# Performance work log

Measured on AMD Instinct MI355X. Metric: run time of the kernel, lower is better.

## Reference

```python
import jax, jax.numpy as jnp
import numpy as np

B, S, D, E, H, TOPK = 4, 1024, 512, 8, 1536, 2
NORM_EPS = 1e-5

def _ln(x, w, b, eps=1e-5):
    m = jnp.mean(x, -1, keepdims=True)
    v = jnp.var(x, -1, keepdims=True)  # biased var, as torch LayerNorm
    return (x - m) * jax.lax.rsqrt(v + eps) * w + b

def _modulate(x, shift, scale):
    return x * (1 + scale[:, None, :]) + shift[:, None, :]

def setup_inputs() -> dict:
    key = jax.random.key(0)
    ks = jax.random.split(key, 14)
    s = 0.02
    return dict(
        x=jax.random.normal(ks[0], (B, S, D), jnp.float32),
        c=jax.random.normal(ks[1], (B, D), jnp.float32),
        W_ada=jax.random.normal(ks[2], (D, 6 * D), jnp.float32) * s,
        b_ada=jax.random.normal(ks[3], (6 * D,), jnp.float32) * 0.1,
        Wq=jax.random.normal(ks[4], (D, D), jnp.float32) * s,
        Wk=jax.random.normal(ks[5], (D, D), jnp.float32) * s,
        Wv=jax.random.normal(ks[6], (D, D), jnp.float32) * s,
        Wo=jax.random.normal(ks[7], (D, D), jnp.float32) * s,
        qn_w=jnp.ones((D,), jnp.float32), qn_b=jnp.zeros((D,), jnp.float32),
        kn_w=jnp.ones((D,), jnp.float32), kn_b=jnp.zeros((D,), jnp.float32),
        an_w=jnp.ones((D,), jnp.float32), an_b=jnp.zeros((D,), jnp.float32),
        fn_w=jnp.ones((D,), jnp.float32), fn_b=jnp.zeros((D,), jnp.float32),
        Wr=jax.random.normal(ks[8], (D, E), jnp.float32) * s,
        br=jnp.zeros((E,), jnp.float32),
        W1=jax.random.normal(ks[9], (E, D, H), jnp.float32) * s,
        W2=jax.random.normal(ks[10], (E, H, D), jnp.float32) * s,
        W3=jax.random.normal(ks[11], (E, D, H), jnp.float32) * s,
    )

def reference(x, c, W_ada, b_ada, Wq, Wk, Wv, Wo, qn_w, qn_b, kn_w, kn_b,
              an_w, an_b, fn_w, fn_b, Wr, br, W1, W2, W3):
    # adaLN conditioning: SiLU -> Linear -> 6 chunks
    mods = jax.nn.silu(c) @ W_ada + b_ada          # (B, 6D)
    sh_msa, sc_msa, g_msa, sh_mlp, sc_mlp, g_mlp = jnp.split(mods, 6, axis=1)

    # Attention (source attends over the FEATURE dim: scores are (B, D, D))
    h = _modulate(_ln(x, an_w, an_b, NORM_EPS), sh_msa, sc_msa)
    q = _ln(h @ Wq, qn_w, qn_b)
    k = _ln(h @ Wk, kn_w, kn_b)
    v = h @ Wv
    scores = jnp.einsum('bsd,bse->bde', q, k)      # (B, D, D), no 1/sqrt scale (as source)
    A = jax.nn.softmax(scores, axis=-1)
    attn = jnp.einsum('bde,bse->bsd', A, v) @ Wo   # (B, S, D)
    x = x + g_msa[:, None, :] * attn

    # MoE feed-forward (top-2 routing; output REPLACES x, no residual/gate per source)
    xm = _modulate(_ln(x, fn_w, fn_b, NORM_EPS), sh_mlp, sc_mlp)
    logits = xm @ Wr + br                          # (B, S, E)
    # F.normalize default dim=1 -> L2 normalize over the SEQUENCE axis (faithful)
    nrm = jnp.sqrt(jnp.sum(logits * logits, axis=1, keepdims=True))
    logits = logits / jnp.maximum(nrm, 1e-12)
    probs = jax.nn.softmax(logits, axis=-1)        # (B, S, E)
    vals, idx = jax.lax.top_k(probs, TOPK)

    T = B * S
    xf = xm.reshape(T, D)
    # dense combine weights: zero for unselected experts (same math as gather/scatter-add)
    wden = jnp.zeros((T, E), xf.dtype).at[jnp.arange(T)[:, None], idx.reshape(T, TOPK)].set(vals.reshape(T, TOPK))
    h1 = jnp.einsum('td,edh->teh', xf, W1)
    h3 = jnp.einsum('td,edh->teh', xf, W3)
    y = jnp.einsum('teh,ehd->ted', jnp.sin(h1) * h3, W2)  # sin-gated FFN per expert
    moe = jnp.einsum('ted,te->td', y, wden).reshape(B, S, D)

    avg = probs.mean(axis=0)                       # mean over batch dim only (faithful): (S, E)
    aux = jnp.sum((1.0 / E - avg) ** 2)
    return moe, aux
```

## Files before the change

### kernel.cpp

```cpp
#include <hip/hip_runtime.h>
#include <math.h>

#define NB 4
#define NS 1024
#define ND 512
#define NE 8
#define NH 1536
#define NT 4096
#define D6 3072

typedef _Float16 half_t;
typedef _Float16 f16x8 __attribute__((ext_vector_type(8)));
typedef _Float16 f16x4 __attribute__((ext_vector_type(4)));
typedef float    f32x4 __attribute__((ext_vector_type(4)));

#define LDC 136
#define TM_MAX 71

__device__ __forceinline__ void gld16(const void* g, void* l) {
  __builtin_amdgcn_global_load_lds((const __attribute__((address_space(1))) char*)g,
                                   (__attribute__((address_space(3))) char*)l, 16, 0, 0);
}

__device__ __forceinline__ int resolve_tile(const int* __restrict__ offs, int t,
                                            int& e_out, int& m0_out) {
  int acc = 0, found = 0, ee = 0, mm = 0;
  #pragma unroll
  for (int q = 0; q < NE; ++q) {
    int ne_q = offs[q + 1] - offs[q];
    int te = (ne_q + 127) >> 7;
    if (!found && t < acc + te) { ee = q; mm = (t - acc) << 7; found = 1; }
    acc += te;
  }
  e_out = ee; m0_out = mm;
  return found;
}

__global__ __launch_bounds__(256) void k_ada(const float* __restrict__ c,
    const float* __restrict__ Wada, const float* __restrict__ bada,
    float* __restrict__ mods)
{
  __shared__ float sc[ND];
  __shared__ float part[256];
  int tid = threadIdx.x;
  int blk = blockIdx.x;
  int o0 = blk * 64;
  int b = o0 / D6;
  int j0 = o0 - b * D6;
  for (int d = tid; d < ND; d += 256) {
    float v = c[b * ND + d];
    sc[d] = v / (1.f + expf(-v));
  }
  __syncthreads();
  int j = j0 + (tid & 63);
  int kc = tid >> 6;
  float acc = 0.f;
  #pragma unroll 8
  for (int d = kc * 128; d < kc * 128 + 128; ++d)
    acc += sc[d] * Wada[(size_t)d * D6 + j];
  part[tid] = acc;
  __syncthreads();
  if (tid < 64) {
    float r = part[tid] + part[tid + 64] + part[tid + 128] + part[tid + 192]
            + bada[j0 + tid];
    mods[b * D6 + j0 + tid] = r;
  }
}

__global__ __launch_bounds__(256) void k_lnmod(const float* X, int xstride,
    float* Yf, half_t* Yh, half_t* Yl, int ystride,
    const float* __restrict__ w, const float* __restrict__ b,
    const float* __restrict__ mods, int sh_off, int sc_off,
    const float* __restrict__ Wr, const float* __restrict__ br,
    float* __restrict__ logits)
{
  __shared__ float red[16];
  __shared__ float red2[32];
  int tid = threadIdx.x;
  int row = blockIdx.x;
  int batch = row >> 10;
  const float* xr = X + (size_t)row * xstride;
  float x0 = xr[tid], x1 = xr[tid + 256];
  float s = x0 + x1, q = x0 * x0 + x1 * x1;
  #pragma unroll
  for (int off = 32; off > 0; off >>= 1) { s += __shfl_down(s, off, 64); q += __shfl_down(q, off, 64); }
  if ((tid & 63) == 0) { red[tid >> 6] = s; red[8 + (tid >> 6)] = q; }
  __syncthreads();
  if (tid == 0) {
    float S = red[0] + red[1] + red[2] + red[3];
    float Q = red[8] + red[9] + red[10] + red[11];
    float mean = S * (1.f / (float)ND);
    float var = Q * (1.f / (float)ND) - mean * mean;
    red[0] = mean; red[1] = rsqrtf(var + 1e-5f);
  }
  __syncthreads();
  float mean = red[0], rstd = red[1];
  int d0 = tid, d1 = tid + 256;
  float y0 = (x0 - mean) * rstd * w[d0] + b[d0];
  float y1 = (x1 - mean) * rstd * w[d1] + b[d1];
  if (mods) {
    const float* mb = mods + batch * D6;
    y0 = y0 * (1.f + mb[sc_off + d0]) + mb[sh_off + d0];
    y1 = y1 * (1.f + mb[sc_off + d1]) + mb[sh_off + d1];
  }
  size_t o0 = (size_t)row * ystride + d0, o1 = (size_t)row * ystride + d1;
  if (Yf) { Yf[o0] = y0; Yf[o1] = y1; }
  if (Yh) {
    half_t h0 = (half_t)y0, h1 = (half_t)y1;
    Yh[o0] = h0; Yh[o1] = h1;
    if (Yl) { Yl[o0] = (half_t)(y0 - (float)h0); Yl[o1] = (half_t)(y1 - (float)h1); }
  }
  if (Wr) {
    float p[8];
    float4 wa = *(const float4*)(Wr + d0 * 8);
    float4 wb = *(const float4*)(Wr + d0 * 8 + 4);
    float4 wc = *(const float4*)(Wr + d1 * 8);
    float4 wd = *(const float4*)(Wr + d1 * 8 + 4);
    p[0] = y0 * wa.x + y1 * wc.x; p[1] = y0 * wa.y + y1 * wc.y;
    p[2] = y0 * wa.z + y1 * wc.z; p[3] = y0 * wa.w + y1 * wc.w;
    p[4] = y0 * wb.x + y1 * wd.x; p[5] = y0 * wb.y + y1 * wd.y;
    p[6] = y0 * wb.z + y1 * wd.z; p[7] = y0 * wb.w + y1 * wd.w;
    #pragma unroll
    for (int off = 32; off > 0; off >>= 1)
      #pragma unroll
      for (int e = 0; e < 8; ++e) p[e] += __shfl_down(p[e], off, 64);
    if ((tid & 63) == 0) {
      #pragma unroll
      for (int e = 0; e < 8; ++e) red2[(tid >> 6) * 8 + e] = p[e];
    }
    __syncthreads();
    if (tid < 8)
      logits[(size_t)row * 8 + tid] = red2[tid] + red2[8 + tid] + red2[16 + tid]
                                    + red2[24 + tid] + br[tid];
  }
}

__global__ __launch_bounds__(256) void k_lnqk(float* QKV,
    const float* __restrict__ qw, const float* __restrict__ qb,
    const float* __restrict__ kw, const float* __restrict__ kb)
{
  __shared__ float red[16];
  int tid = threadIdx.x;
  int row = blockIdx.x >> 1;
  int h = blockIdx.x & 1;
  const float* w = h ? kw : qw;
  const float* b = h ? kb : qb;
  float* xr = QKV + (size_t)row * 1536 + h * 512;
  float x0 = xr[tid], x1 = xr[tid + 256];
  float s = x0 + x1, q = x0 * x0 + x1 * x1;
  #pragma unroll
  for (int off = 32; off > 0; off >>= 1) { s += __shfl_down(s, off, 64); q += __shfl_down(q, off, 64); }
  if ((tid & 63) == 0) { red[tid >> 6] = s; red[8 + (tid >> 6)] = q; }
  __syncthreads();
  if (tid == 0) {
    float S = red[0] + red[1] + red[2] + red[3];
    float Q = red[8] + red[9] + red[10] + red[11];
    float mean = S * (1.f / (float)ND);
    float var = Q * (1.f / (float)ND) - mean * mean;
    red[0] = mean; red[1] = rsqrtf(var + 1e-5f);
  }
  __syncthreads();
  float mean = red[0], rstd = red[1];
  xr[tid]       = (x0 - mean) * rstd * w[tid] + b[tid];
  xr[tid + 256] = (x1 - mean) * rstd * w[tid + 256] + b[tid + 256];
}

__global__ __launch_bounds__(256) void k_tsplit2(const float* __restrict__ QKV,
    half_t* __restrict__ H0, half_t* __restrict__ L0)
{
  __shared__ float tile[32][33];
  int z = blockIdx.z;
  half_t* outH = H0 + (size_t)z * 4194304;
  half_t* outL = L0 + (size_t)z * 4194304;
  int col0 = z * 512;
  int s0 = blockIdx.x * 32, c0 = blockIdx.y * 32;
  int tid = threadIdx.x;
  int r = tid >> 5, c = tid & 31;
  #pragma unroll
  for (int p = 0; p < 4; ++p)
    tile[r + p * 8][c] = QKV[(size_t)(s0 + r + p * 8) * 1536 + col0 + c0 + c];
  __syncthreads();
  #pragma unroll
  for (int p = 0; p < 4; ++p) {
    float v = tile[c][r + p * 8];
    half_t h = (half_t)v;
    size_t o = (size_t)(c0 + r + p * 8) * NT + s0 + c;
    outH[o] = h; outL[o] = (half_t)(v - (float)h);
  }
}

__global__ __launch_bounds__(256) void k_wsplit4(const float* __restrict__ Wq,
    const float* __restrict__ Wk, const float* __restrict__ Wv,
    const float* __restrict__ Wo, half_t* __restrict__ outH, half_t* __restrict__ outL)
{
  __shared__ float tile[32][33];
  int z = blockIdx.z;
  const float* W = (z == 0) ? Wq : (z == 1) ? Wk : (z == 2) ? Wv : Wo;
  int rowoff = z * 512;
  int k0 = blockIdx.x * 32, n0 = blockIdx.y * 32;
  int tid = threadIdx.x;
  int r = tid >> 5, c = tid & 31;
  #pragma unroll
  for (int p = 0; p < 4; ++p)
    tile[r + p * 8][c] = W[(size_t)(k0 + r + p * 8) * ND + n0 + c];
  __syncthreads();
  #pragma unroll
  for (int p = 0; p < 4; ++p) {
    float v = tile[c][r + p * 8];
    half_t h = (half_t)v;
    size_t o = (size_t)(rowoff + n0 + r + p * 8) * ND + k0 + c;
    outH[o] = h; outL[o] = (half_t)(v - (float)h);
  }
}

__global__ __launch_bounds__(256) void k_vsplit(const float* __restrict__ QKV,
    half_t* __restrict__ Vh, half_t* __restrict__ Vl)
{
  int i = blockIdx.x * 256 + threadIdx.x;
  int s = i >> 7, c = (i & 127) * 4;
  float4 v = *(const float4*)(QKV + (size_t)s * 1536 + 1024 + c);
  f16x4 h, l;
  h[0] = (half_t)v.x; l[0] = (half_t)(v.x - (float)h[0]);
  h[1] = (half_t)v.y; l[1] = (half_t)(v.y - (float)h[1]);
  h[2] = (half_t)v.z; l[2] = (half_t)(v.z - (float)h[2]);
  h[3] = (half_t)v.w; l[3] = (half_t)(v.w - (float)h[3]);
  *(f16x4*)(Vh + (size_t)s * ND + c) = h;
  *(f16x4*)(Vl + (size_t)s * ND + c) = l;
}

template<int MODE>
__global__ __launch_bounds__(256, 2) void k_gemm_hl(
    const half_t* __restrict__ Ah, const half_t* __restrict__ Al, long long sAz,
    const half_t* __restrict__ Bh, const half_t* __restrict__ Bl, long long sBz,
    int lda, int ldb, int K,
    float* __restrict__ Cf, half_t* __restrict__ Ch, half_t* __restrict__ Cl,
    long long sCz, int ldc,
    const float* __restrict__ xres, const float* __restrict__ mods)
{
  int z = blockIdx.z;
  int m0 = blockIdx.x * 128, n0 = blockIdx.y * 128;
  __shared__ __align__(16) char smem[65536];
  half_t* Sh = (half_t*)smem;
  int tid = threadIdx.x;
  int lane = tid & 63, w = tid >> 6;
  int wm = (w >> 1) * 64, wn = (w & 1) * 64;
  int qd = lane >> 4, md = lane & 15;
  int rA0 = tid >> 2;
  int sw = (((tid & 3) ^ ((tid >> 3) & 3)) << 3);

  const half_t* pAh0 = Ah + z * sAz + (size_t)(m0 + rA0) * lda + sw;
  const half_t* pAh1 = pAh0 + (size_t)64 * lda;
  const half_t* pAl0 = Al + z * sAz + (size_t)(m0 + rA0) * lda + sw;
  const half_t* pAl1 = pAl0 + (size_t)64 * lda;
  const half_t* pBh0 = Bh + z * sBz + (size_t)(n0 + rA0) * ldb + sw;
  const half_t* pBh1 = pBh0 + (size_t)64 * ldb;
  const half_t* pBl0 = Bl + z * sBz + (size_t)(n0 + rA0) * ldb + sw;
  const half_t* pBl1 = pBl0 + (size_t)64 * ldb;

  char* dAh = smem + w * 1024;
  char* dAl = smem + 16384 + w * 1024;
  char* dBh = smem + 32768 + w * 1024;
  char* dBl = smem + 49152 + w * 1024;

  f32x4 acc[4][4];
  #pragma unroll
  for (int i = 0; i < 4; ++i)
    #pragma unroll
    for (int j = 0; j < 4; ++j)
      #pragma unroll
      for (int p = 0; p < 4; ++p) acc[i][j][p] = 0.f;

  int swq  = ((qd ^ ((md >> 1) & 3)) << 3);
  int aoff = (wm + md) * 32 + swq;
  int boff = (wn + md) * 32 + swq;

#define GEMM_STAGE(p, kk) do { int kb_ = (kk); int pb_ = (p) * 8192;         \
    gld16(pAh0 + kb_, dAh + pb_); gld16(pAh1 + kb_, dAh + pb_ + 4096);       \
    gld16(pAl0 + kb_, dAl + pb_); gld16(pAl1 + kb_, dAl + pb_ + 4096);       \
    gld16(pBh0 + kb_, dBh + pb_); gld16(pBh1 + kb_, dBh + pb_ + 4096);       \
    gld16(pBl0 + kb_, dBl + pb_); gld16(pBl1 + kb_, dBl + pb_ + 4096); } while (0)

  int iters = K >> 5;
  GEMM_STAGE(0, 0);
  int cur = 0;
  #pragma unroll 1
  for (int it = 0; it < iters; ++it) {
    if (it + 1 < iters) {
      GEMM_STAGE(cur ^ 1, (it + 1) * 32);
      asm volatile("s_waitcnt vmcnt(8)\ns_barrier" ::: "memory");
    } else {
      asm volatile("s_waitcnt vmcnt(0)\ns_barrier" ::: "memory");
    }
    const half_t* Ash = Sh + cur * 4096;
    const half_t* Asl = Sh + 8192  + cur * 4096;
    const half_t* Bsh = Sh + 16384 + cur * 4096;
    const half_t* Bsl = Sh + 24576 + cur * 4096;
    f16x8 ah[4], al[4], bh[4], bl[4];
    #pragma unroll
    for (int i = 0; i < 4; ++i) {
      ah[i] = *(const f16x8*)(Ash + aoff + i * 512);
      al[i] = *(const f16x8*)(Asl + aoff + i * 512);
    }
    #pragma unroll
    for (int j = 0; j < 4; ++j) {
      bh[j] = *(const f16x8*)(Bsh + boff + j * 512);
      bl[j] = *(const f16x8*)(Bsl + boff + j * 512);
    }
    __builtin_amdgcn_s_setprio(1);
    #pragma unroll
    for (int i = 0; i < 4; ++i)
      #pragma unroll
      for (int j = 0; j < 4; ++j) {
        acc[i][j] = __builtin_amdgcn_mfma_f32_16x16x32_f16(ah[i], bh[j], acc[i][j], 0, 0, 0);
        acc[i][j] = __builtin_amdgcn_mfma_f32_16x16x32_f16(ah[i], bl[j], acc[i][j], 0, 0, 0);
        acc[i][j] = __builtin_amdgcn_mfma_f32_16x16x32_f16(al[i], bh[j], acc[i][j], 0, 0, 0);
      }
    __builtin_amdgcn_s_setprio(0);
    asm volatile("s_barrier" ::: "memory");
    cur ^= 1;
  }
#undef GEMM_STAGE

  if (MODE == 1) {
    half_t* Cs = (half_t*)smem;
    __syncthreads();
    #pragma unroll
    for (int i = 0; i < 4; ++i)
      #pragma unroll
      for (int j = 0; j < 4; ++j)
        #pragma unroll
        for (int p = 0; p < 4; ++p)
          Cs[(wm + 16 * i + qd * 4 + p) * LDC + wn + 16 * j + md] = (half_t)acc[i][j][p];
    __syncthreads();
    #pragma unroll
    for (int it2 = 0; it2 < 8; ++it2) {
      int chunk = it2 * 256 + tid;
      int r = chunk >> 4, c8 = (chunk & 15) * 8;
      *(f16x8*)(Ch + z * sCz + (size_t)(m0 + r) * ldc + n0 + c8) = *(const f16x8*)(Cs + r * LDC + c8);
    }
    __syncthreads();
    #pragma unroll
    for (int i = 0; i < 4; ++i)
      #pragma unroll
      for (int j = 0; j < 4; ++j)
        #pragma unroll
        for (int p = 0; p < 4; ++p) {
          float v = acc[i][j][p];
          half_t h = (half_t)v;
          Cs[(wm + 16 * i + qd * 4 + p) * LDC + wn + 16 * j + md] = (half_t)(v - (float)h);
        }
    __syncthreads();
    #pragma unroll
    for (int it2 = 0; it2 < 8; ++it2) {
      int chunk = it2 * 256 + tid;
      int r = chunk >> 4, c8 = (chunk & 15) * 8;
      *(f16x8*)(Cl + z * sCz + (size_t)(m0 + r) * ldc + n0 + c8) = *(const f16x8*)(Cs + r * LDC + c8);
    }
  } else {
    #pragma unroll
    for (int i = 0; i < 4; ++i)
      #pragma unroll
      for (int p = 0; p < 4; ++p) {
        int r = m0 + wm + 16 * i + qd * 4 + p;
        float* cp = Cf + z * sCz + (size_t)r * ldc + n0 + wn + md;
        if (MODE == 2) {
          int batch = r >> 10;
          const float* mb = mods + batch * D6 + 2 * ND;
          const float* xp = xres + (size_t)r * ldc + n0 + wn + md;
          #pragma unroll
          for (int j = 0; j < 4; ++j) {
            int col = wn + md + 16 * j;
            cp[16 * j] = xp[16 * j] + mb[n0 + col] * acc[i][j][p];
          }
        } else {
          #pragma unroll
          for (int j = 0; j < 4; ++j) cp[16 * j] = acc[i][j][p];
        }
      }
  }
}

__global__ __launch_bounds__(256) void k_softmax512_sum4(const float* __restrict__ SC4,
    half_t* __restrict__ Ph, half_t* __restrict__ Pl)
{
  __shared__ float red[16];
  int tid = threadIdx.x;
  int row = blockIdx.x;
  int b = row >> 9, d = row & 511;
  const float* r0 = SC4 + ((size_t)(b * 4 + 0) << 18) + (size_t)d * ND;
  const float* r1 = SC4 + ((size_t)(b * 4 + 1) << 18) + (size_t)d * ND;
  const float* r2 = SC4 + ((size_t)(b * 4 + 2) << 18) + (size_t)d * ND;
  const float* r3 = SC4 + ((size_t)(b * 4 + 3) << 18) + (size_t)d * ND;
  float x0 = r0[tid] + r1[tid] + r2[tid] + r3[tid];
  float x1 = r0[tid + 256] + r1[tid + 256] + r2[tid + 256] + r3[tid + 256];
  float m = fmaxf(x0, x1);
  #pragma unroll
  for (int off = 32; off > 0; off >>= 1) m = fmaxf(m, __shfl_down(m, off, 64));
  if ((tid & 63) == 0) red[tid >> 6] = m;
  __syncthreads();
  if (tid == 0) red[0] = fmaxf(fmaxf(red[0], red[1]), fmaxf(red[2], red[3]));
  __syncthreads();
  m = red[0];
  float e0 = expf(x0 - m), e1 = expf(x1 - m);
  float s = e0 + e1;
  #pragma unroll
  for (int off = 32; off > 0; off >>= 1) s += __shfl_down(s, off, 64);
  if ((tid & 63) == 0) red[8 + (tid >> 6)] = s;
  __syncthreads();
  if (tid == 0) red[8] = red[8] + red[9] + red[10] + red[11];
  __syncthreads();
  float inv = 1.f / red[8];
  float p0 = e0 * inv, p1 = e1 * inv;
  size_t base = (size_t)row * ND;
  half_t h0 = (half_t)p0, h1 = (half_t)p1;
  Ph[base + tid] = h0;       Pl[base + tid] = (half_t)(p0 - (float)h0);
  Ph[base + tid + 256] = h1; Pl[base + tid + 256] = (half_t)(p1 - (float)h1);
}

__global__ __launch_bounds__(256) void k_colnorm(const float* __restrict__ logits,
    float* __restrict__ nrm, int* __restrict__ cnt)
{
  __shared__ float red[8];
  int tid = threadIdx.x;
  if (blockIdx.x == 0 && tid < 16) cnt[tid] = 0;
  int b = blockIdx.x >> 3, e = blockIdx.x & 7;
  float acc = 0.f;
  for (int s = tid; s < NS; s += 256) {
    float l = logits[((size_t)(b << 10) + s) * NE + e];
    acc += l * l;
  }
  #pragma unroll
  for (int off = 32; off > 0; off >>= 1) acc += __shfl_down(acc, off, 64);
  if ((tid & 63) == 0) red[tid >> 6] = acc;
  __syncthreads();
  if (tid == 0) nrm[b * NE + e] = sqrtf(red[0] + red[1] + red[2] + red[3]);
}

__global__ __launch_bounds__(256) void k_top2(const float* __restrict__ logits,
    const float* __restrict__ nrm, float* __restrict__ probs,
    float* __restrict__ wsel, int* __restrict__ isel, int* __restrict__ cnt)
{
  int t = blockIdx.x * 256 + threadIdx.x;
  int b = t >> 10;
  float p[NE];
  float mx = -1e30f;
  #pragma unroll
  for (int e = 0; e < NE; ++e) {
    float l = logits[t * NE + e] / fmaxf(nrm[b * NE + e], 1e-12f);
    p[e] = l;
    mx = fmaxf(mx, l);
  }
  float s = 0.f;
  #pragma unroll
  for (int e = 0; e < NE; ++e) { p[e] = expf(p[e] - mx); s += p[e]; }
  float inv = 1.f / s;
  #pragma unroll
  for (int e = 0; e < NE; ++e) { p[e] *= inv; probs[t * NE + e] = p[e]; }
  int i1 = 0;
  #pragma unroll
  for (int e = 1; e < NE; ++e) if (p[e] > p[i1]) i1 = e;
  int i2 = (i1 == 0) ? 1 : 0;
  #pragma unroll
  for (int e = 0; e < NE; ++e) if (e != i1 && p[e] > p[i2]) i2 = e;
  wsel[t * 2] = p[i1]; wsel[t * 2 + 1] = p[i2];
  isel[t * 2] = i1;    isel[t * 2 + 1] = i2;
  atomicAdd(&cnt[i1], 1); atomicAdd(&cnt[i2], 1);
}

__global__ void k_scan(const int* __restrict__ cnt, int* __restrict__ offs)
{
  if (threadIdx.x == 0) {
    int a = 0;
    for (int e = 0; e < NE; ++e) { offs[e] = a; a += cnt[e]; }
    offs[NE] = a;
  }
}

__global__ __launch_bounds__(256) void k_fill(const int* __restrict__ isel,
    const int* __restrict__ offs, int* __restrict__ cnt2,
    int* __restrict__ list, int* __restrict__ inv)
{
  int idx = blockIdx.x * 256 + threadIdx.x;
  int e = isel[idx];
  int pos = atomicAdd(&cnt2[e], 1);
  int slot = offs[e] + pos;
  list[slot] = idx >> 1;
  inv[idx] = slot;
}

__global__ __launch_bounds__(256) void k_aux(const float* __restrict__ probs,
    float* __restrict__ outAux)
{
  __shared__ float red[8];
  int tid = threadIdx.x;
  float acc = 0.f;
  for (int s = tid; s < NS; s += 256) {
    #pragma unroll
    for (int e = 0; e < NE; ++e) {
      float a = probs[(size_t)s * NE + e] + probs[(size_t)(NS + s) * NE + e]
              + probs[(size_t)(2 * NS + s) * NE + e] + probs[(size_t)(3 * NS + s) * NE + e];
      float d = 0.125f - a * 0.25f;
      acc += d * d;
    }
  }
  #pragma unroll
  for (int off = 32; off > 0; off >>= 1) acc += __shfl_down(acc, off, 64);
  if ((tid & 63) == 0) red[tid >> 6] = acc;
  __syncthreads();
  if (tid == 0) *outAux = red[0] + red[1] + red[2] + red[3];
}

__global__ __launch_bounds__(256) void k_tcast13(const float* __restrict__ W1,
    const float* __restrict__ W3, half_t* __restrict__ W1t, half_t* __restrict__ W3t)
{
  __shared__ float tile[32][33];
  int z = blockIdx.z;
  int sel = z >> 3, e = z & 7;
  const float* We = (sel ? W3 : W1) + (size_t)e * ND * NH;
  half_t* Wte = (sel ? W3t : W1t) + (size_t)e * ND * NH;
  int k0 = blockIdx.x * 32, n0 = blockIdx.y * 32;
  int tid = threadIdx.x;
  int r = tid >> 5, c = tid & 31;
  #pragma unroll
  for (int p = 0; p < 4; ++p)
    tile[r + p * 8][c] = We[(size_t)(k0 + r + p * 8) * NH + n0 + c];
  __syncthreads();
  #pragma unroll
  for (int p = 0; p < 4; ++p)
    Wte[(size_t)(n0 + r + p * 8) * ND + k0 + c] = (half_t)tile[c][r + p * 8];
}

__global__ __launch_bounds__(256) void k_tcastW2(const float* __restrict__ W,
    half_t* __restrict__ Wt)
{
  __shared__ float tile[32][33];
  const float* We = W + (size_t)blockIdx.z * NH * ND;
  half_t* Wte = Wt + (size_t)blockIdx.z * NH * ND;
  int k0 = blockIdx.x * 32, n0 = blockIdx.y * 32;
  int tid = threadIdx.x;
  int r = tid >> 5, c = tid & 31;
  #pragma unroll
  for (int p = 0; p < 4; ++p)
    tile[r + p * 8][c] = We[(size_t)(k0 + r + p * 8) * ND + n0 + c];
  __syncthreads();
  #pragma unroll
  for (int p = 0; p < 4; ++p)
    Wte[(size_t)(n0 + r + p * 8) * NH + k0 + c] = (half_t)tile[c][r + p * 8];
}

__global__ __launch_bounds__(256, 3) void k_ffn_fused(const half_t* __restrict__ xmh,
    const half_t* __restrict__ W1t, const half_t* __restrict__ W3t,
    const int* __restrict__ list, const int* __restrict__ offs,
    half_t* __restrict__ gate)
{
  int bx = blockIdx.x;
  int n0 = (bx % 12) * 128;
  int t  = bx / 12;
  int e, m0;
  if (!resolve_tile(offs, t, e, m0)) return;
  int base = offs[e], ne = offs[e + 1] - base;

  __shared__ __align__(16) char smem[49664];
  half_t* Sh = (half_t*)smem;
  int* rowt = (int*)(smem + 49152);
  int tid = threadIdx.x;
  if (tid < 128) {
    int rr = m0 + tid;
    rowt[tid] = (rr < ne) ? list[base + rr] : 0;
  }
  __syncthreads();

  int lane = tid & 63, w = tid >> 6;
  int wm = (w >> 1) * 64, wn = (w & 1) * 64;
  int qd = lane >> 4, md = lane & 15;
  int rA0 = tid >> 2;
  int sw = (((tid & 3) ^ ((tid >> 3) & 3)) << 3);
  int tok0 = rowt[rA0], tok1 = rowt[rA0 + 64];

  const half_t* gA0  = xmh + (size_t)tok0 * ND + sw;
  const half_t* gA1  = xmh + (size_t)tok1 * ND + sw;
  const half_t* gB10 = W1t + ((size_t)e * NH + n0 + rA0) * ND + sw;
  const half_t* gB11 = gB10 + (size_t)64 * ND;
  const half_t* gB30 = W3t + ((size_t)e * NH + n0 + rA0) * ND + sw;
  const half_t* gB31 = gB30 + (size_t)64 * ND;

  char* dA  = smem + w * 1024;
  char* dB1 = smem + 16384 + w * 1024;
  char* dB3 = smem + 32768 + w * 1024;

  f32x4 acc1[4][4], acc3[4][4];
  #pragma unroll
  for (int i = 0; i < 4; ++i)
    #pragma unroll
    for (int j = 0; j < 4; ++j)
      #pragma unroll
      for (int p = 0; p < 4; ++p) { acc1[i][j][p] = 0.f; acc3[i][j][p] = 0.f; }

  int swq  = ((qd ^ ((md >> 1) & 3)) << 3);
  int aoff = (wm + md) * 32 + swq;
  int boff = (wn + md) * 32 + swq;

#define FFN_STAGE(p, kk) do { int kb_ = (kk); int pb_ = (p) * 8192;          \
    gld16(gA0  + kb_, dA  + pb_); gld16(gA1  + kb_, dA  + pb_ + 4096);       \
    gld16(gB10 + kb_, dB1 + pb_); gld16(gB11 + kb_, dB1 + pb_ + 4096);       \
    gld16(gB30 + kb_, dB3 + pb_); gld16(gB31 + kb_, dB3 + pb_ + 4096); } while (0)

  FFN_STAGE(0, 0);
  int cur = 0;
  #pragma unroll 1
  for (int it = 0; it < 16; ++it) {
    if (it + 1 < 16) {
      FFN_STAGE(cur ^ 1, (it + 1) * 32);
      asm volatile("s_waitcnt vmcnt(6)\ns_barrier" ::: "memory");
    } else {
      asm volatile("s_waitcnt vmcnt(0)\ns_barrier" ::: "memory");
    }
    const half_t* As  = Sh + cur * 4096;
    const half_t* B1s = Sh + 8192  + cur * 4096;
    const half_t* B3s = Sh + 16384 + cur * 4096;
    f16x8 a[4];
    #pragma unroll
    for (int i = 0; i < 4; ++i) a[i] = *(const f16x8*)(As + aoff + i * 512);
    __builtin_amdgcn_s_setprio(1);
    #pragma unroll
    for (int j = 0; j < 4; ++j) {
      f16x8 b1 = *(const f16x8*)(B1s + boff + j * 512);
      f16x8 b3 = *(const f16x8*)(B3s + boff + j * 512);
      #pragma unroll
      for (int i = 0; i < 4; ++i) {
        acc1[i][j] = __builtin_amdgcn_mfma_f32_16x16x32_f16(a[i], b1, acc1[i][j], 0, 0, 0);
        acc3[i][j] = __builtin_amdgcn_mfma_f32_16x16x32_f16(a[i], b3, acc3[i][j], 0, 0, 0);
      }
    }
    __builtin_amdgcn_s_setprio(0);
    asm volatile("s_barrier" ::: "memory");
    cur ^= 1;
  }
#undef FFN_STAGE

  half_t* Cs = (half_t*)smem;
  #pragma unroll
  for (int i = 0; i < 4; ++i)
    #pragma unroll
    for (int j = 0; j < 4; ++j)
      #pragma unroll
      for (int p = 0; p < 4; ++p) {
        int rr = wm + 16 * i + qd * 4 + p;
        int cc = wn + 16 * j + md;
        Cs[rr * LDC + cc] = (half_t)(__sinf(acc1[i][j][p]) * acc3[i][j][p]);
      }
  __syncthreads();
  #pragma unroll
  for (int it = 0; it < 8; ++it) {
    int chunk = it * 256 + tid;
    int rr = chunk >> 4, c8 = (chunk & 15) * 8;
    if (m0 + rr < ne) {
      *(f16x8*)(gate + (size_t)(base + m0 + rr) * NH + n0 + c8) = *(const f16x8*)(Cs + rr * LDC + c8);
    }
  }
}

__global__ __launch_bounds__(256, 4) void k_moe2_mfma(const half_t* __restrict__ gate,
    const half_t* __restrict__ W2t, const int* __restrict__ offs,
    float* __restrict__ P)
{
  int bx = blockIdx.x;
  int n0 = (bx & 3) * 128;
  int t = bx >> 2;
  int e, m0;
  if (!resolve_tile(offs, t, e, m0)) return;
  int base = offs[e], ne = offs[e + 1] - base;

  __shared__ __align__(16) char smem[32768];
  half_t* Sh = (half_t*)smem;
  int tid = threadIdx.x;
  int lane = tid & 63, w = tid >> 6;
  int wm = (w >> 1) * 64, wn = (w & 1) * 64;
  int qd = lane >> 4, md = lane & 15;
  int rA0 = tid >> 2;
  int sw = (((tid & 3) ^ ((tid >> 3) & 3)) << 3);

  int ar0 = m0 + rA0;      if (ar0 >= ne) ar0 = ne - 1;
  int ar1 = m0 + rA0 + 64; if (ar1 >= ne) ar1 = ne - 1;
  const half_t* gA0 = gate + (size_t)(base + ar0) * NH + sw;
  const half_t* gA1 = gate + (size_t)(base + ar1) * NH + sw;
  const half_t* gB0 = W2t + ((size_t)e * ND + n0 + rA0) * NH + sw;
  const half_t* gB1 = gB0 + (size_t)64 * NH;

  char* dA = smem + w * 1024;
  char* dB = smem + 16384 + w * 1024;

  f32x4 acc[4][4];
  #pragma unroll
  for (int i = 0; i < 4; ++i)
    #pragma unroll
    for (int j = 0; j < 4; ++j)
      #pragma unroll
      for (int p = 0; p < 4; ++p) acc[i][j][p] = 0.f;

  int swq  = ((qd ^ ((md >> 1) & 3)) << 3);
  int aoff = (wm + md) * 32 + swq;
  int boff = (wn + md) * 32 + swq;

#define MOE2_STAGE(p, kk) do { int kb_ = (kk); int pb_ = (p) * 8192;         \
    gld16(gA0 + kb_, dA + pb_); gld16(gA1 + kb_, dA + pb_ + 4096);           \
    gld16(gB0 + kb_, dB + pb_); gld16(gB1 + kb_, dB + pb_ + 4096); } while (0)

  MOE2_STAGE(0, 0);
  int cur = 0;
  #pragma unroll 1
  for (int it = 0; it < 48; ++it) {
    if (it + 1 < 48) {
      MOE2_STAGE(cur ^ 1, (it + 1) * 32);
      asm volatile("s_waitcnt vmcnt(4)\ns_barrier" ::: "memory");
    } else {
      asm volatile("s_waitcnt vmcnt(0)\ns_barrier" ::: "memory");
    }
    const half_t* As = Sh + cur * 4096;
    const half_t* Bs = Sh + 8192 + cur * 4096;
    f16x8 a[4];
    #pragma unroll
    for (int i = 0; i < 4; ++i) a[i] = *(const f16x8*)(As + aoff + i * 512);
    __builtin_amdgcn_s_setprio(1);
    #pragma unroll
    for (int j = 0; j < 4; ++j) {
      f16x8 b = *(const f16x8*)(Bs + boff + j * 512);
      #pragma unroll
      for (int i = 0; i < 4; ++i)
        acc[i][j] = __builtin_amdgcn_mfma_f32_16x16x32_f16(a[i], b, acc[i][j], 0, 0, 0);
    }
    __builtin_amdgcn_s_setprio(0);
    asm volatile("s_barrier" ::: "memory");
    cur ^= 1;
  }
#undef MOE2_STAGE

  #pragma unroll
  for (int i = 0; i < 4; ++i)
    #pragma unroll
    for (int p = 0; p < 4; ++p) {
      int gr = m0 + wm + 16 * i + qd * 4 + p;
      if (gr < ne) {
        float* pp = P + (size_t)(base + gr) * ND + n0 + wn + md;
        #pragma unroll
        for (int j = 0; j < 4; ++j)
          pp[16 * j] = acc[i][j][p];
      }
    }
}

__global__ __launch_bounds__(256) void k_moe_reduce(const float* __restrict__ P,
    const int* __restrict__ inv, const float* __restrict__ wsel,
    float* __restrict__ out)
{
  int i = blockIdx.x * 256 + threadIdx.x;
  int t = i >> 7, d4 = i & 127;
  int s1 = inv[t * 2], s2 = inv[t * 2 + 1];
  float w1 = wsel[t * 2], w2 = wsel[t * 2 + 1];
  const float4* P4 = (const float4*)P;
  float4 a = P4[(size_t)s1 * 128 + d4];
  float4 b = P4[(size_t)s2 * 128 + d4];
  float4 o;
  o.x = w1 * a.x + w2 * b.x;
  o.y = w1 * a.y + w2 * b.y;
  o.z = w1 * a.z + w2 * b.z;
  o.w = w1 * a.w + w2 * b.w;
  ((float4*)out)[i] = o;
}

static const size_t BO_MODS  = 0;
static const size_t BO_HH    = 65536;
static const size_t BO_HL2   = 4259840;
static const size_t BO_PH    = 4259840;
static const size_t BO_PL    = 6357056;
static const size_t BO_WALLH = 8454144;
static const size_t BO_WALLL = 10551296;
static const size_t BO_QKV   = 12648448;
static const size_t BO_A0H   = 12648448;
static const size_t BO_A0L   = 16842752;
static const size_t BO_SC4   = 21037056;
static const size_t BO_X2    = 21037056;
static const size_t BO_XM    = 29425664;
static const size_t BO_QTH   = 37814272;
static const size_t BO_QTL   = 42008576;
static const size_t BO_KTH   = 46202880;
static const size_t BO_KTL   = 50397184;
static const size_t BO_VH    = 54591488;
static const size_t BO_VL    = 58785792;
static const size_t BO_W1T   = 37814272;
static const size_t BO_XMH   = 50397184;
static const size_t BO_W3T   = 65536;
static const size_t BO_GATE  = 12648448;
static const size_t BO_W2T   = 65536;
static const size_t BO_P     = 37814272;
static const size_t BO_LOGI  = 62980096;
static const size_t BO_NRM   = 63111168;
static const size_t BO_PROB  = 63111296;
static const size_t BO_WSEL  = 63242368;
static const size_t BO_INTS  = 63307904;

extern "C" void kernel_launch(void* const* d_in, const int* in_sizes, int n_in,
                              void* d_out, int out_size, void* d_ws, size_t ws_size,
                              hipStream_t stream)
{
  const float* x    = (const float*)d_in[0];
  const float* c    = (const float*)d_in[1];
  const float* Wada = (const float*)d_in[2];
  const float* bada = (const float*)d_in[3];
  const float* Wq   = (const float*)d_in[4];
  const float* Wk   = (const float*)d_in[5];
  const float* Wv   = (const float*)d_in[6];
  const float* Wo   = (const float*)d_in[7];
  const float* qn_w = (const float*)d_in[8];
  const float* qn_b = (const float*)d_in[9];
  const float* kn_w = (const float*)d_in[10];
  const float* kn_b = (const float*)d_in[11];
  const float* an_w = (const float*)d_in[12];
  const float* an_b = (const float*)d_in[13];
  const float* fn_w = (const float*)d_in[14];
  const float* fn_b = (const float*)d_in[15];
  const float* Wr   = (const float*)d_in[16];
  const float* br   = (const float*)d_in[17];
  const float* W1   = (const float*)d_in[18];
  const float* W2   = (const float*)d_in[19];
  const float* W3   = (const float*)d_in[20];
  float* out = (float*)d_out;
  char*  ws8 = (char*)d_ws;
  float* MODS = (float*)(ws8 + BO_MODS);
  half_t* Hh = (half_t*)(ws8 + BO_HH),   *Hl = (half_t*)(ws8 + BO_HL2);
  half_t* Ph = (half_t*)(ws8 + BO_PH),   *Pl = (half_t*)(ws8 + BO_PL);
  half_t* WALLH = (half_t*)(ws8 + BO_WALLH), *WALLL = (half_t*)(ws8 + BO_WALLL);
  half_t* WoTh = WALLH + (size_t)1536 * ND,  *WoTl = WALLL + (size_t)1536 * ND;
  float* QKV = (float*)(ws8 + BO_QKV);
  half_t* A0h = (half_t*)(ws8 + BO_A0H), *A0l = (half_t*)(ws8 + BO_A0L);
  float* SC4 = (float*)(ws8 + BO_SC4);
  float* X2  = (float*)(ws8 + BO_X2);
  float* XM  = (float*)(ws8 + BO_XM);
  half_t* qTh = (half_t*)(ws8 + BO_QTH), *qTl = (half_t*)(ws8 + BO_QTL);
  half_t* kTh = (half_t*)(ws8 + BO_KTH), *kTl = (half_t*)(ws8 + BO_KTL);
  half_t* Vh  = (half_t*)(ws8 + BO_VH),  *Vl  = (half_t*)(ws8 + BO_VL);
  half_t* W1T = (half_t*)(ws8 + BO_W1T);
  half_t* W3T = (half_t*)(ws8 + BO_W3T);
  half_t* W2T = (half_t*)(ws8 + BO_W2T);
  half_t* XMH = (half_t*)(ws8 + BO_XMH);
  half_t* GATEH = (half_t*)(ws8 + BO_GATE);
  float* PBUF = (float*)(ws8 + BO_P);
  float* LOGI = (float*)(ws8 + BO_LOGI);
  float* NRM  = (float*)(ws8 + BO_NRM);
  float* PROB = (float*)(ws8 + BO_PROB);
  float* WSEL = (float*)(ws8 + BO_WSEL);
  int* ib   = (int*)(ws8 + BO_INTS);
  int* isel = ib;
  int* cnt  = ib + 8192;
  int* cnt2 = ib + 8200;
  int* offs = ib + 8208;
  int* list = ib + 8224;
  int* inv  = ib + 16416;

  k_ada<<<192, 256, 0, stream>>>(c, Wada, bada, MODS);
  k_wsplit4<<<dim3(16, 16, 4), 256, 0, stream>>>(Wq, Wk, Wv, Wo, WALLH, WALLL);
  k_lnmod<<<NT, 256, 0, stream>>>(x, ND, nullptr, Hh, Hl, ND, an_w, an_b, MODS, 0, 512,
                                  nullptr, nullptr, nullptr);
  k_gemm_hl<0><<<dim3(32, 12, 1), 256, 0, stream>>>(Hh, Hl, 0, WALLH, WALLL, 0,
      ND, ND, ND, QKV, nullptr, nullptr, 0, 1536, nullptr, nullptr);
  k_lnqk<<<2 * NT, 256, 0, stream>>>(QKV, qn_w, qn_b, kn_w, kn_b);
  k_tsplit2<<<dim3(128, 16, 2), 256, 0, stream>>>(QKV, qTh, qTl);
  k_vsplit<<<2048, 256, 0, stream>>>(QKV, Vh, Vl);
  k_gemm_hl<0><<<dim3(4, 4, 16), 256, 0, stream>>>(qTh, qTl, 256, kTh, kTl, 256,
      NT, NT, 256, SC4, nullptr, nullptr, 262144, ND, nullptr, nullptr);
  k_softmax512_sum4<<<2048, 256, 0, stream>>>(SC4, Ph, Pl);
  k_gemm_hl<1><<<dim3(8, 4, 4), 256, 0, stream>>>(Vh, Vl, 524288, Ph, Pl, 262144,
      ND, ND, ND, nullptr, A0h, A0l, 524288, ND, nullptr, nullptr);
  k_gemm_hl<2><<<dim3(32, 4, 1), 256, 0, stream>>>(A0h, A0l, 0, WoTh, WoTl, 0,
      ND, ND, ND, X2, nullptr, nullptr, 0, ND, x, MODS);
  k_lnmod<<<NT, 256, 0, stream>>>(X2, ND, XM, XMH, nullptr, ND, fn_w, fn_b, MODS, 1536, 2048,
                                  Wr, br, LOGI);
  k_colnorm<<<32, 256, 0, stream>>>(LOGI, NRM, cnt);
  k_top2<<<16, 256, 0, stream>>>(LOGI, NRM, PROB, WSEL, isel, cnt);
  k_scan<<<1, 64, 0, stream>>>(cnt, offs);
  k_fill<<<32, 256, 0, stream>>>(isel, offs, cnt2, list, inv);
  k_aux<<<1, 256, 0, stream>>>(PROB, out + (size_t)NT * ND);
  k_tcast13<<<dim3(16, 48, 16), 256, 0, stream>>>(W1, W3, W1T, W3T);
  k_ffn_fused<<<TM_MAX * 12, 256, 0, stream>>>(XMH, W1T, W3T, list, offs, GATEH);
  k_tcastW2<<<dim3(48, 16, 8), 256, 0, stream>>>(W2, W2T);
  k_moe2_mfma<<<TM_MAX * 4, 256, 0, stream>>>(GATEH, W2T, offs, PBUF);
  k_moe_reduce<<<2048, 256, 0, stream>>>(PBUF, inv, WSEL, out);
}
```

Before: 452.2 us.

## Fuse top-2 routing, scan and fill into one single-block kernel

Replaces the top2, scan and fill kernels with a single 1024-thread block that computes softmax and top-2 for all tokens, builds per-expert counts with wave ballots, prefix-scans them in shared memory and writes the list and inverse slots. This removes two kernel launches and the global atomic counters, and makes slot order deterministic. In exchange the routing work runs on one block (one CU) with serial loops instead of spread over many blocks.

```diff
diff --git a/kernel.cpp b/kernel.cpp
--- a/kernel.cpp
+++ b/kernel.cpp
@@ -418,11 +418,10 @@
 }
 
 __global__ __launch_bounds__(256) void k_colnorm(const float* __restrict__ logits,
-    float* __restrict__ nrm, int* __restrict__ cnt)
+    float* __restrict__ nrm)
 {
   __shared__ float red[8];
   int tid = threadIdx.x;
-  if (blockIdx.x == 0 && tid < 16) cnt[tid] = 0;
   int b = blockIdx.x >> 3, e = blockIdx.x & 7;
   float acc = 0.f;
   for (int s = tid; s < NS; s += 256) {
@@ -436,56 +435,88 @@
   if (tid == 0) nrm[b * NE + e] = sqrtf(red[0] + red[1] + red[2] + red[3]);
 }
 
-__global__ __launch_bounds__(256) void k_top2(const float* __restrict__ logits,
+__global__ __launch_bounds__(1024) void k_route(const float* __restrict__ logits,
     const float* __restrict__ nrm, float* __restrict__ probs,
-    float* __restrict__ wsel, int* __restrict__ isel, int* __restrict__ cnt)
-{
-  int t = blockIdx.x * 256 + threadIdx.x;
-  int b = t >> 10;
-  float p[NE];
-  float mx = -1e30f;
-  #pragma unroll
-  for (int e = 0; e < NE; ++e) {
-    float l = logits[t * NE + e] / fmaxf(nrm[b * NE + e], 1e-12f);
-    p[e] = l;
-    mx = fmaxf(mx, l);
-  }
-  float s = 0.f;
-  #pragma unroll
-  for (int e = 0; e < NE; ++e) { p[e] = expf(p[e] - mx); s += p[e]; }
-  float inv = 1.f / s;
-  #pragma unroll
-  for (int e = 0; e < NE; ++e) { p[e] *= inv; probs[t * NE + e] = p[e]; }
-  int i1 = 0;
-  #pragma unroll
-  for (int e = 1; e < NE; ++e) if (p[e] > p[i1]) i1 = e;
-  int i2 = (i1 == 0) ? 1 : 0;
-  #pragma unroll
-  for (int e = 0; e < NE; ++e) if (e != i1 && p[e] > p[i2]) i2 = e;
-  wsel[t * 2] = p[i1]; wsel[t * 2 + 1] = p[i2];
-  isel[t * 2] = i1;    isel[t * 2 + 1] = i2;
-  atomicAdd(&cnt[i1], 1); atomicAdd(&cnt[i2], 1);
-}
-
-__global__ void k_scan(const int* __restrict__ cnt, int* __restrict__ offs)
-{
-  if (threadIdx.x == 0) {
+    float* __restrict__ wsel, int* __restrict__ offs_g,
+    int* __restrict__ list, int* __restrict__ inv)
+{
+  __shared__ unsigned char sisel[8192];
+  __shared__ int cw[8][16][8];
+  __shared__ int soffs[9];
+  __shared__ float snrm[32];
+  int tid = threadIdx.x;
+  int lane = tid & 63, wv = tid >> 6;
+  if (tid < 32) snrm[tid] = fmaxf(nrm[tid], 1e-12f);
+  __syncthreads();
+  #pragma unroll 1
+  for (int c = 0; c < 4; ++c) {
+    int t = c * 1024 + tid;
+    int b = t >> 10;
+    float p[8];
+    float4 l0 = *(const float4*)(logits + (size_t)t * 8);
+    float4 l1 = *(const float4*)(logits + (size_t)t * 8 + 4);
+    p[0] = l0.x / snrm[b * 8 + 0]; p[1] = l0.y / snrm[b * 8 + 1];
+    p[2] = l0.z / snrm[b * 8 + 2]; p[3] = l0.w / snrm[b * 8 + 3];
+    p[4] = l1.x / snrm[b * 8 + 4]; p[5] = l1.y / snrm[b * 8 + 5];
+    p[6] = l1.z / snrm[b * 8 + 6]; p[7] = l1.w / snrm[b * 8 + 7];
+    float mx = p[0];
+    #pragma unroll
+    for (int e = 1; e < 8; ++e) mx = fmaxf(mx, p[e]);
+    float s = 0.f;
+    #pragma unroll
+    for (int e = 0; e < 8; ++e) { p[e] = expf(p[e] - mx); s += p[e]; }
+    float invs = 1.f / s;
+    #pragma unroll
+    for (int e = 0; e < 8; ++e) { p[e] *= invs; probs[(size_t)t * 8 + e] = p[e]; }
+    int i1 = 0;
+    #pragma unroll
+    for (int e = 1; e < 8; ++e) if (p[e] > p[i1]) i1 = e;
+    int i2 = (i1 == 0) ? 1 : 0;
+    #pragma unroll
+    for (int e = 0; e < 8; ++e) if (e != i1 && p[e] > p[i2]) i2 = e;
+    wsel[t * 2] = p[i1]; wsel[t * 2 + 1] = p[i2];
+    sisel[t * 2] = (unsigned char)i1; sisel[t * 2 + 1] = (unsigned char)i2;
+  }
+  __syncthreads();
+  #pragma unroll 1
+  for (int c = 0; c < 8; ++c) {
+    int em = sisel[c * 1024 + tid];
+    #pragma unroll
+    for (int e = 0; e < 8; ++e) {
+      unsigned long long mask = __ballot(em == e);
+      if (lane == 0) cw[c][wv][e] = (int)__popcll(mask);
+    }
+  }
+  __syncthreads();
+  if (tid < 8) {
+    int e = tid, run = 0;
+    for (int c = 0; c < 8; ++c)
+      for (int w2 = 0; w2 < 16; ++w2) { int v = cw[c][w2][e]; cw[c][w2][e] = run; run += v; }
+    soffs[e] = run;
+  }
+  __syncthreads();
+  if (tid == 0) {
     int a = 0;
-    for (int e = 0; e < NE; ++e) { offs[e] = a; a += cnt[e]; }
-    offs[NE] = a;
-  }
-}
-
-__global__ __launch_bounds__(256) void k_fill(const int* __restrict__ isel,
-    const int* __restrict__ offs, int* __restrict__ cnt2,
-    int* __restrict__ list, int* __restrict__ inv)
-{
-  int idx = blockIdx.x * 256 + threadIdx.x;
-  int e = isel[idx];
-  int pos = atomicAdd(&cnt2[e], 1);
-  int slot = offs[e] + pos;
-  list[slot] = idx >> 1;
-  inv[idx] = slot;
+    #pragma unroll
+    for (int e = 0; e < 8; ++e) { int v = soffs[e]; soffs[e] = a; a += v; }
+    soffs[8] = a;
+  }
+  __syncthreads();
+  if (tid < 9) offs_g[tid] = soffs[tid];
+  #pragma unroll 1
+  for (int c = 0; c < 8; ++c) {
+    int idx = c * 1024 + tid;
+    int em = sisel[idx];
+    int rk = 0;
+    #pragma unroll
+    for (int e = 0; e < 8; ++e) {
+      unsigned long long mask = __ballot(em == e);
+      if (em == e) rk = (int)__popcll(mask & ((1ull << lane) - 1ull));
+    }
+    int slot = soffs[em] + cw[c][wv][em] + rk;
+    list[slot] = idx >> 1;
+    inv[idx] = slot;
+  }
 }
 
 __global__ __launch_bounds__(256) void k_aux(const float* __restrict__ probs,
@@ -850,9 +881,6 @@
   float* PROB = (float*)(ws8 + BO_PROB);
   float* WSEL = (float*)(ws8 + BO_WSEL);
   int* ib   = (int*)(ws8 + BO_INTS);
-  int* isel = ib;
-  int* cnt  = ib + 8192;
-  int* cnt2 = ib + 8200;
   int* offs = ib + 8208;
   int* list = ib + 8224;
   int* inv  = ib + 16416;
@@ -875,10 +903,8 @@
       ND, ND, ND, X2, nullptr, nullptr, 0, ND, x, MODS);
   k_lnmod<<<NT, 256, 0, stream>>>(X2, ND, XM, XMH, nullptr, ND, fn_w, fn_b, MODS, 1536, 2048,
                                   Wr, br, LOGI);
-  k_colnorm<<<32, 256, 0, stream>>>(LOGI, NRM, cnt);
-  k_top2<<<16, 256, 0, stream>>>(LOGI, NRM, PROB, WSEL, isel, cnt);
-  k_scan<<<1, 64, 0, stream>>>(cnt, offs);
-  k_fill<<<32, 256, 0, stream>>>(isel, offs, cnt2, list, inv);
+  k_colnorm<<<32, 256, 0, stream>>>(LOGI, NRM);
+  k_route<<<1, 1024, 0, stream>>>(LOGI, NRM, PROB, WSEL, offs, list, inv);
   k_aux<<<1, 256, 0, stream>>>(PROB, out + (size_t)NT * ND);
   k_tcast13<<<dim3(16, 48, 16), 256, 0, stream>>>(W1, W3, W1T, W3T);
   k_ffn_fused<<<TM_MAX * 12, 256, 0, stream>>>(XMH, W1T, W3T, list, offs, GATEH);
```

Result: faster. 394.8 us (-12.7%).
